# Optimization experiments

Hardware: AMD Instinct MI355X
Metric: run time of the kernel (lower is better)

Reference implementation:

```python
import jax, jax.numpy as jnp
import numpy as np

B, L, C = 1, 4096, 1024
H = 16
D = C // H  # head_dim = 64


def setup_inputs() -> dict:
    key = jax.random.key(0)
    k1, k2, k3 = jax.random.split(key, 3)
    scale_in = 1.0 / np.sqrt(C)
    return {
        "x": jax.random.normal(k1, (B, L, C), dtype=jnp.float32),
        "Wqkv": jax.random.normal(k2, (C, 3 * C), dtype=jnp.float32) * scale_in,
        "bqkv": jnp.zeros((3 * C,), dtype=jnp.float32),
        "Wout": jax.random.normal(k3, (C, C), dtype=jnp.float32) * scale_in,
        "bout": jnp.zeros((C,), dtype=jnp.float32),
    }


def reference(x, Wqkv, bqkv, Wout, bout):
    Bx, Lx, Cx = x.shape
    qkv = x @ Wqkv + bqkv                             # [B, L, 3C]
    qkv = qkv.reshape(Bx, Lx, 3, H, D)
    qkv = jnp.transpose(qkv, (2, 0, 3, 1, 4))         # [3, B, H, L, D]
    q, k, v = qkv[0], qkv[1], qkv[2]
    scores = jnp.einsum("bhqd,bhkd->bhqk", q, k) / jnp.sqrt(jnp.float32(D))
    # causal mask: strictly upper triangle -> -inf
    causal = jnp.triu(jnp.ones((Lx, Lx), dtype=bool), k=1)
    scores = jnp.where(causal, -jnp.inf, scores)
    attn = jax.nn.softmax(scores, axis=-1)            # [B, H, L, L]
    out = jnp.einsum("bhqk,bhkd->bhqd", attn, v)      # [B, H, L, D]
    out = jnp.transpose(out, (0, 2, 1, 3)).reshape(Bx, Lx, Cx)
    return out @ Wout + bout
```

## Files before the change

kernel.cpp:

```cpp
#include <hip/hip_runtime.h>
#include <hip/hip_bf16.h>

typedef unsigned short u16;
typedef __bf16 bf16x8 __attribute__((ext_vector_type(8)));
typedef float f32x4 __attribute__((ext_vector_type(4)));

#define L_SEQ 4096
#define CDIM  1024
#define NH    16
#define HD    64
#define N_QKV 3072
#define ATT_STRIDE 88

static __device__ __forceinline__ float bf2f(u16 u) {
    union { float f; unsigned int i; } v; v.i = ((unsigned int)u) << 16; return v.f;
}
static __device__ __forceinline__ u16 f2bf(float f) {
    union { float f; unsigned int i; } v; v.f = f;
    unsigned int u = v.i;
    return (u16)((u + 0x7fffu + ((u >> 16) & 1u)) >> 16);
}

static __device__ __forceinline__ f32x4 mfma16x16x32(bf16x8 a, bf16x8 b, f32x4 c) {
    return __builtin_amdgcn_mfma_f32_16x16x32_bf16(a, b, c, 0, 0, 0);
}

typedef const __attribute__((address_space(1))) unsigned int* gas_u32;
typedef __attribute__((address_space(3))) unsigned int* las_u32;
static __device__ __forceinline__ void gload_lds16(const u16* g, u16* l) {
    __builtin_amdgcn_global_load_lds((gas_u32)g, (las_u32)l, 16, 0, 0);
}

__global__ __launch_bounds__(256) void k_cast_x(const float* __restrict__ src,
                                                u16* __restrict__ dst, int n8) {
    int i = blockIdx.x * 256 + threadIdx.x;
    if (i >= n8) return;
    const float4* s = (const float4*)(src + (size_t)i * 8);
    float4 a = s[0], b = s[1];
    u16 o[8] = { f2bf(a.x), f2bf(a.y), f2bf(a.z), f2bf(a.w),
                 f2bf(b.x), f2bf(b.y), f2bf(b.z), f2bf(b.w) };
    *(uint4*)(dst + (size_t)i * 8) = *(uint4*)o;
}

__global__ __launch_bounds__(256) void k_transpose_cast(const float* __restrict__ src,
                                                        u16* __restrict__ dst,
                                                        int R, int C) {
    __shared__ u16 tile[32][33];
    int c0 = blockIdx.x * 32, r0 = blockIdx.y * 32;
    int tx = threadIdx.x & 31, ty = threadIdx.x >> 5;
#pragma unroll
    for (int i = 0; i < 32; i += 8)
        tile[ty + i][tx] = f2bf(src[(size_t)(r0 + ty + i) * C + c0 + tx]);
    __syncthreads();
#pragma unroll
    for (int i = 0; i < 32; i += 8)
        dst[(size_t)(c0 + ty + i) * R + r0 + tx] = tile[tx][ty + i];
}

__global__ __launch_bounds__(256) void k_transpose_v(const u16* __restrict__ qkv,
                                                     u16* __restrict__ vt) {
    __shared__ u16 tile[32][33];
    int k0 = blockIdx.x * 32, d0 = blockIdx.y * 32, h = blockIdx.z;
    int tx = threadIdx.x & 31, ty = threadIdx.x >> 5;
#pragma unroll
    for (int i = 0; i < 32; i += 8)
        tile[ty + i][tx] = qkv[(size_t)(k0 + ty + i) * N_QKV + 2 * CDIM + h * HD + d0 + tx];
    __syncthreads();
#pragma unroll
    for (int i = 0; i < 32; i += 8)
        vt[(size_t)(h * HD + d0 + ty + i) * L_SEQ + k0 + tx] = tile[tx][ty + i];
}

template <typename OutT>
__global__ __launch_bounds__(256) void k_gemm_bt(const u16* __restrict__ A,
                                                 const u16* __restrict__ Bt,
                                                 const float* __restrict__ bias,
                                                 OutT* __restrict__ Cmat,
                                                 int M, int N, int K) {
    __shared__ alignas(16) u16 As[128 * 32];
    __shared__ alignas(16) u16 Bs[128 * 32];
    int t = threadIdx.x;
    int n0 = blockIdx.x * 128, m0 = blockIdx.y * 128;
    int l = t & 63, w = t >> 6;
    int wm = (w >> 1) * 64, wn = (w & 1) * 64;
    int lr = l & 15, lq = l >> 4;

    const f32x4 vzero = {0.f, 0.f, 0.f, 0.f};
    f32x4 acc[4][4];
#pragma unroll
    for (int mi = 0; mi < 4; mi++)
#pragma unroll
        for (int ni = 0; ni < 4; ni++) acc[mi][ni] = vzero;

    int ar = t >> 2;
    int ac = (t & 3) * 8;
    const u16* Ag = A + (size_t)(m0 + ar) * K + ac;
    const u16* Bg = Bt + (size_t)(n0 + ar) * K + ac;
    u16* AsD0 = &As[t * 8];
    u16* AsD1 = &As[t * 8 + 64 * 32];
    u16* BsD0 = &Bs[t * 8];
    u16* BsD1 = &Bs[t * 8 + 64 * 32];

    for (int k0 = 0; k0 < K; k0 += 32) {
        gload_lds16(Ag + k0,                     AsD0);
        gload_lds16(Ag + (size_t)64 * K + k0,    AsD1);
        gload_lds16(Bg + k0,                     BsD0);
        gload_lds16(Bg + (size_t)64 * K + k0,    BsD1);
        __syncthreads();

        bf16x8 af[4], bfr[4];
#pragma unroll
        for (int mi = 0; mi < 4; mi++)
            af[mi] = *(const bf16x8*)&As[(wm + mi * 16 + lr) * 32 + lq * 8];
#pragma unroll
        for (int ni = 0; ni < 4; ni++)
            bfr[ni] = *(const bf16x8*)&Bs[(wn + ni * 16 + lr) * 32 + lq * 8];
#pragma unroll
        for (int mi = 0; mi < 4; mi++)
#pragma unroll
            for (int ni = 0; ni < 4; ni++)
                acc[mi][ni] = mfma16x16x32(af[mi], bfr[ni], acc[mi][ni]);
        __syncthreads();
    }

#pragma unroll
    for (int ni = 0; ni < 4; ni++) {
        int col = n0 + wn + ni * 16 + lr;
        float bv = bias[col];
#pragma unroll
        for (int mi = 0; mi < 4; mi++) {
            int row = m0 + wm + mi * 16 + lq * 4;
#pragma unroll
            for (int r = 0; r < 4; r++) {
                float v = acc[mi][ni][r] + bv;
                if constexpr (sizeof(OutT) == 2)
                    Cmat[(size_t)(row + r) * N + col] = f2bf(v);
                else
                    Cmat[(size_t)(row + r) * N + col] = v;
            }
        }
    }
}

__global__ __launch_bounds__(256) void k_attn(const u16* __restrict__ qkv,
                                              const u16* __restrict__ vt,
                                              u16* __restrict__ attn) {
    __shared__ alignas(16) u16 Ks[64 * ATT_STRIDE];
    __shared__ alignas(16) u16 Vs[64 * ATT_STRIDE];

    int t = threadIdx.x;
    int l = t & 63, w = t >> 6;
    int h = blockIdx.y;
    int lr = l & 15, lq = l >> 4;
    int row8 = t >> 3;
    int ch = (t & 7) * 8;
    int qloc = w * 16 + lr;

    const f32x4 vzero = {0.f, 0.f, 0.f, 0.f};
    const u16* Kbase = qkv + (size_t)row8 * N_QKV + CDIM + h * HD + ch;
    const u16* Vbase = vt + (size_t)(h * HD + row8) * L_SEQ + ch;

#pragma unroll
    for (int phase = 0; phase < 2; phase++) {
        int tile = phase ? (63 - blockIdx.x) : blockIdx.x;
        int q0 = tile * 64;
        int nkv = tile + 1;

        bf16x8 bq[2];
        {
            const u16* Qg = qkv + (size_t)(q0 + qloc) * N_QKV + h * HD + lq * 8;
            union { uint4 u; u16 hh[8]; } q0u, q1u;
            q0u.u = *(const uint4*)(Qg);
            q1u.u = *(const uint4*)(Qg + 32);
            union { bf16x8 v; u16 hh[8]; } f0, f1;
#pragma unroll
            for (int j = 0; j < 8; j++) {
                f0.hh[j] = f2bf(bf2f(q0u.hh[j]) * 0.125f);
                f1.hh[j] = f2bf(bf2f(q1u.hh[j]) * 0.125f);
            }
            bq[0] = f0.v; bq[1] = f1.v;
        }

        f32x4 o[4];
#pragma unroll
        for (int dt = 0; dt < 4; dt++) o[dt] = vzero;
        float m_i = -1e30f, l_i = 0.f;

        uint4 rk0, rk1, rv0, rv1;
        {
            const u16* Kg = Kbase;
            rk0 = *(const uint4*)Kg;
            rk1 = *(const uint4*)(Kg + (size_t)32 * N_QKV);
            const u16* Vg = Vbase;
            rv0 = *(const uint4*)Vg;
            rv1 = *(const uint4*)(Vg + (size_t)32 * L_SEQ);
        }

        for (int it = 0; it < nkv; ++it) {
            *(uint4*)&Ks[row8 * ATT_STRIDE + ch]        = rk0;
            *(uint4*)&Ks[(row8 + 32) * ATT_STRIDE + ch] = rk1;
            *(uint4*)&Vs[row8 * ATT_STRIDE + ch]        = rv0;
            *(uint4*)&Vs[(row8 + 32) * ATT_STRIDE + ch] = rv1;
            __syncthreads();

            if (it + 1 < nkv) {
                int k1 = (it + 1) * 64;
                const u16* Kg = Kbase + (size_t)k1 * N_QKV;
                rk0 = *(const uint4*)Kg;
                rk1 = *(const uint4*)(Kg + (size_t)32 * N_QKV);
                const u16* Vg = Vbase + k1;
                rv0 = *(const uint4*)Vg;
                rv1 = *(const uint4*)(Vg + (size_t)32 * L_SEQ);
            }

            f32x4 s[4];
#pragma unroll
            for (int nt = 0; nt < 4; nt++) s[nt] = vzero;
#pragma unroll
            for (int ks = 0; ks < 2; ks++)
#pragma unroll
                for (int nt = 0; nt < 4; nt++) {
                    bf16x8 ak = *(const bf16x8*)&Ks[(nt * 16 + lr) * ATT_STRIDE + ks * 32 + lq * 8];
                    s[nt] = mfma16x16x32(ak, bq[ks], s[nt]);
                }

            bool diag = ((it * 64) == q0);
            float tmax = -1e30f;
#pragma unroll
            for (int nt = 0; nt < 4; nt++)
#pragma unroll
                for (int r = 0; r < 4; r++) {
                    float v = s[nt][r];
                    if (diag && (nt * 16 + lq * 4 + r > qloc)) v = -1e30f;
                    s[nt][r] = v;
                    tmax = fmaxf(tmax, v);
                }
            tmax = fmaxf(tmax, __shfl_xor(tmax, 16));
            tmax = fmaxf(tmax, __shfl_xor(tmax, 32));

            float mnew = fmaxf(m_i, tmax);
            float alpha = __expf(m_i - mnew);
            float rsum = 0.f;
#pragma unroll
            for (int nt = 0; nt < 4; nt++)
#pragma unroll
                for (int r = 0; r < 4; r++) {
                    float e = __expf(s[nt][r] - mnew);
                    s[nt][r] = e;
                    rsum += e;
                }
            rsum += __shfl_xor(rsum, 16);
            rsum += __shfl_xor(rsum, 32);
            l_i = l_i * alpha + rsum;
            m_i = mnew;
#pragma unroll
            for (int dt = 0; dt < 4; dt++)
#pragma unroll
                for (int r = 0; r < 4; r++) o[dt][r] *= alpha;

#pragma unroll
            for (int a = 0; a < 2; a++) {
                union { bf16x8 v; u16 hh[8]; } bp;
#pragma unroll
                for (int r = 0; r < 4; r++) {
                    bp.hh[r]     = f2bf(s[2 * a][r]);
                    bp.hh[r + 4] = f2bf(s[2 * a + 1][r]);
                }
#pragma unroll
                for (int dt = 0; dt < 4; dt++) {
                    union { bf16x8 v; uint2 u2[2]; } av;
                    const u16* vrow = &Vs[(dt * 16 + lr) * ATT_STRIDE + a * 32 + lq * 4];
                    av.u2[0] = *(const uint2*)(vrow);
                    av.u2[1] = *(const uint2*)(vrow + 16);
                    o[dt] = mfma16x16x32(av.v, bp.v, o[dt]);
                }
            }
            __syncthreads();
        }

        float inv = 1.0f / l_i;
        int qg = q0 + qloc;
#pragma unroll
        for (int dt = 0; dt < 4; dt++) {
            union { u16 hh[4]; uint2 u2; } eo;
#pragma unroll
            for (int r = 0; r < 4; r++) eo.hh[r] = f2bf(o[dt][r] * inv);
            *(uint2*)&attn[(size_t)qg * CDIM + h * HD + dt * 16 + lq * 4] = eo.u2;
        }
    }
}

extern "C" void kernel_launch(void* const* d_in, const int* in_sizes, int n_in,
                              void* d_out, int out_size, void* d_ws, size_t ws_size,
                              hipStream_t stream) {
    const float* x    = (const float*)d_in[0];
    const float* Wqkv = (const float*)d_in[1];
    const float* bqkv = (const float*)d_in[2];
    const float* Wout = (const float*)d_in[3];
    const float* bout = (const float*)d_in[4];
    float* out = (float*)d_out;

    char* ws = (char*)d_ws;
    u16* qkv   = (u16*)(ws);
    u16* xb    = (u16*)(ws + 25165824);
    u16* attn  = xb;
    u16* vt    = (u16*)(ws + 33554432);
    u16* wqkvt = (u16*)(ws + 41943040);
    u16* woutt = (u16*)(ws + 48234496);

    k_cast_x<<<dim3(2048), 256, 0, stream>>>(x, xb, 524288);
    k_transpose_cast<<<dim3(96, 32), 256, 0, stream>>>(Wqkv, wqkvt, 1024, 3072);
    k_transpose_cast<<<dim3(32, 32), 256, 0, stream>>>(Wout, woutt, 1024, 1024);
    k_gemm_bt<u16><<<dim3(24, 32), 256, 0, stream>>>(xb, wqkvt, bqkv, qkv, 4096, 3072, 1024);
    k_transpose_v<<<dim3(128, 2, 16), 256, 0, stream>>>(qkv, vt);
    k_attn<<<dim3(32, 16), 256, 0, stream>>>(qkv, vt, attn);
    k_gemm_bt<float><<<dim3(8, 32), 256, 0, stream>>>(attn, woutt, bout, out, 4096, 1024, 1024);
}
```

Measured before the change: 246.9 us.

## Split attention KV range across two warp groups and merge softmax partials

The attention kernel now launches 512 threads per block. Two groups of four waves each process half of the KV tiles for the same query tile, each with its own shared-memory K/V buffers. The partial max, sum and output accumulators are then merged through shared memory in a flash-decoding style combine. This doubles the parallelism per query tile, since the grid of 512 blocks underfills the GPU. The cost is an extra merge step, block-wide syncs shared by both groups, and idle iterations for the group with fewer tiles.

After: 236.6 us. 1.04x faster.

```diff
diff --git a/kernel.cpp b/kernel.cpp
--- a/kernel.cpp
+++ b/kernel.cpp
@@ -142,29 +142,37 @@
     }
 }
 
-__global__ __launch_bounds__(256) void k_attn(const u16* __restrict__ qkv,
-                                              const u16* __restrict__ vt,
-                                              u16* __restrict__ attn) {
-    __shared__ alignas(16) u16 Ks[64 * ATT_STRIDE];
-    __shared__ alignas(16) u16 Vs[64 * ATT_STRIDE];
+__global__ __launch_bounds__(512, 4) void k_attn(const u16* __restrict__ qkv,
+                                                 const u16* __restrict__ vt,
+                                                 u16* __restrict__ attn) {
+    __shared__ alignas(16) u16 Ks[2][64 * ATT_STRIDE];
+    __shared__ alignas(16) u16 Vs[2][64 * ATT_STRIDE];
 
     int t = threadIdx.x;
     int l = t & 63, w = t >> 6;
+    int g = w >> 2;
+    int ww = w & 3;
     int h = blockIdx.y;
     int lr = l & 15, lq = l >> 4;
-    int row8 = t >> 3;
-    int ch = (t & 7) * 8;
-    int qloc = w * 16 + lr;
+    int tg = t & 255;
+    int row8 = tg >> 3;
+    int ch = (tg & 7) * 8;
+    int qloc = ww * 16 + lr;
 
     const f32x4 vzero = {0.f, 0.f, 0.f, 0.f};
     const u16* Kbase = qkv + (size_t)row8 * N_QKV + CDIM + h * HD + ch;
     const u16* Vbase = vt + (size_t)(h * HD + row8) * L_SEQ + ch;
+    u16* KsG = Ks[g];
+    u16* VsG = Vs[g];
 
 #pragma unroll
     for (int phase = 0; phase < 2; phase++) {
         int tile = phase ? (63 - blockIdx.x) : blockIdx.x;
         int q0 = tile * 64;
         int nkv = tile + 1;
+        int h0 = (nkv + 1) >> 1;
+        int myBeg = g ? h0 : 0;
+        int myCnt = g ? (nkv - h0) : h0;
 
         bf16x8 bq[2];
         {
@@ -186,25 +194,28 @@
         for (int dt = 0; dt < 4; dt++) o[dt] = vzero;
         float m_i = -1e30f, l_i = 0.f;
 
-        uint4 rk0, rk1, rv0, rv1;
-        {
-            const u16* Kg = Kbase;
+        uint4 rk0 = {0,0,0,0}, rk1 = {0,0,0,0}, rv0 = {0,0,0,0}, rv1 = {0,0,0,0};
+        if (myCnt > 0) {
+            const u16* Kg = Kbase + (size_t)(myBeg * 64) * N_QKV;
             rk0 = *(const uint4*)Kg;
             rk1 = *(const uint4*)(Kg + (size_t)32 * N_QKV);
-            const u16* Vg = Vbase;
+            const u16* Vg = Vbase + myBeg * 64;
             rv0 = *(const uint4*)Vg;
             rv1 = *(const uint4*)(Vg + (size_t)32 * L_SEQ);
         }
 
-        for (int it = 0; it < nkv; ++it) {
-            *(uint4*)&Ks[row8 * ATT_STRIDE + ch]        = rk0;
-            *(uint4*)&Ks[(row8 + 32) * ATT_STRIDE + ch] = rk1;
-            *(uint4*)&Vs[row8 * ATT_STRIDE + ch]        = rv0;
-            *(uint4*)&Vs[(row8 + 32) * ATT_STRIDE + ch] = rv1;
+        for (int it = 0; it < h0; ++it) {
+            bool act = it < myCnt;
+            if (act) {
+                *(uint4*)&KsG[row8 * ATT_STRIDE + ch]        = rk0;
+                *(uint4*)&KsG[(row8 + 32) * ATT_STRIDE + ch] = rk1;
+                *(uint4*)&VsG[row8 * ATT_STRIDE + ch]        = rv0;
+                *(uint4*)&VsG[(row8 + 32) * ATT_STRIDE + ch] = rv1;
+            }
             __syncthreads();
 
-            if (it + 1 < nkv) {
-                int k1 = (it + 1) * 64;
+            if (it + 1 < myCnt) {
+                int k1 = (myBeg + it + 1) * 64;
                 const u16* Kg = Kbase + (size_t)k1 * N_QKV;
                 rk0 = *(const uint4*)Kg;
                 rk1 = *(const uint4*)(Kg + (size_t)32 * N_QKV);
@@ -213,80 +224,111 @@
                 rv1 = *(const uint4*)(Vg + (size_t)32 * L_SEQ);
             }
 
-            f32x4 s[4];
-#pragma unroll
-            for (int nt = 0; nt < 4; nt++) s[nt] = vzero;
-#pragma unroll
-            for (int ks = 0; ks < 2; ks++)
-#pragma unroll
-                for (int nt = 0; nt < 4; nt++) {
-                    bf16x8 ak = *(const bf16x8*)&Ks[(nt * 16 + lr) * ATT_STRIDE + ks * 32 + lq * 8];
-                    s[nt] = mfma16x16x32(ak, bq[ks], s[nt]);
+            if (act) {
+                f32x4 s[4];
+#pragma unroll
+                for (int nt = 0; nt < 4; nt++) s[nt] = vzero;
+#pragma unroll
+                for (int ks = 0; ks < 2; ks++)
+#pragma unroll
+                    for (int nt = 0; nt < 4; nt++) {
+                        bf16x8 ak = *(const bf16x8*)&KsG[(nt * 16 + lr) * ATT_STRIDE + ks * 32 + lq * 8];
+                        s[nt] = mfma16x16x32(ak, bq[ks], s[nt]);
+                    }
+
+                bool diag = (((myBeg + it) * 64) == q0);
+                float tmax = -1e30f;
+#pragma unroll
+                for (int nt = 0; nt < 4; nt++)
+#pragma unroll
+                    for (int r = 0; r < 4; r++) {
+                        float v = s[nt][r];
+                        if (diag && (nt * 16 + lq * 4 + r > qloc)) v = -1e30f;
+                        s[nt][r] = v;
+                        tmax = fmaxf(tmax, v);
+                    }
+                tmax = fmaxf(tmax, __shfl_xor(tmax, 16));
+                tmax = fmaxf(tmax, __shfl_xor(tmax, 32));
+
+                float mnew = fmaxf(m_i, tmax);
+                float alpha = __expf(m_i - mnew);
+                float rsum = 0.f;
+#pragma unroll
+                for (int nt = 0; nt < 4; nt++)
+#pragma unroll
+                    for (int r = 0; r < 4; r++) {
+                        float e = __expf(s[nt][r] - mnew);
+                        s[nt][r] = e;
+                        rsum += e;
+                    }
+                rsum += __shfl_xor(rsum, 16);
+                rsum += __shfl_xor(rsum, 32);
+                l_i = l_i * alpha + rsum;
+                m_i = mnew;
+#pragma unroll
+                for (int dt = 0; dt < 4; dt++)
+#pragma unroll
+                    for (int r = 0; r < 4; r++) o[dt][r] *= alpha;
+
+#pragma unroll
+                for (int a = 0; a < 2; a++) {
+                    union { bf16x8 v; u16 hh[8]; } bp;
+#pragma unroll
+                    for (int r = 0; r < 4; r++) {
+                        bp.hh[r]     = f2bf(s[2 * a][r]);
+                        bp.hh[r + 4] = f2bf(s[2 * a + 1][r]);
+                    }
+#pragma unroll
+                    for (int dt = 0; dt < 4; dt++) {
+                        union { bf16x8 v; uint2 u2[2]; } av;
+                        const u16* vrow = &VsG[(dt * 16 + lr) * ATT_STRIDE + a * 32 + lq * 4];
+                        av.u2[0] = *(const uint2*)(vrow);
+                        av.u2[1] = *(const uint2*)(vrow + 16);
+                        o[dt] = mfma16x16x32(av.v, bp.v, o[dt]);
+                    }
                 }
-
-            bool diag = ((it * 64) == q0);
-            float tmax = -1e30f;
-#pragma unroll
-            for (int nt = 0; nt < 4; nt++)
-#pragma unroll
-                for (int r = 0; r < 4; r++) {
-                    float v = s[nt][r];
-                    if (diag && (nt * 16 + lq * 4 + r > qloc)) v = -1e30f;
-                    s[nt][r] = v;
-                    tmax = fmaxf(tmax, v);
-                }
-            tmax = fmaxf(tmax, __shfl_xor(tmax, 16));
-            tmax = fmaxf(tmax, __shfl_xor(tmax, 32));
-
-            float mnew = fmaxf(m_i, tmax);
-            float alpha = __expf(m_i - mnew);
-            float rsum = 0.f;
-#pragma unroll
-            for (int nt = 0; nt < 4; nt++)
-#pragma unroll
-                for (int r = 0; r < 4; r++) {
-                    float e = __expf(s[nt][r] - mnew);
-                    s[nt][r] = e;
-                    rsum += e;
-                }
-            rsum += __shfl_xor(rsum, 16);
-            rsum += __shfl_xor(rsum, 32);
-            l_i = l_i * alpha + rsum;
-            m_i = mnew;
-#pragma unroll
-            for (int dt = 0; dt < 4; dt++)
-#pragma unroll
-                for (int r = 0; r < 4; r++) o[dt][r] *= alpha;
-
-#pragma unroll
-            for (int a = 0; a < 2; a++) {
-                union { bf16x8 v; u16 hh[8]; } bp;
-#pragma unroll
-                for (int r = 0; r < 4; r++) {
-                    bp.hh[r]     = f2bf(s[2 * a][r]);
-                    bp.hh[r + 4] = f2bf(s[2 * a + 1][r]);
-                }
-#pragma unroll
-                for (int dt = 0; dt < 4; dt++) {
-                    union { bf16x8 v; uint2 u2[2]; } av;
-                    const u16* vrow = &Vs[(dt * 16 + lr) * ATT_STRIDE + a * 32 + lq * 4];
-                    av.u2[0] = *(const uint2*)(vrow);
-                    av.u2[1] = *(const uint2*)(vrow + 16);
-                    o[dt] = mfma16x16x32(av.v, bp.v, o[dt]);
-                }
             }
             __syncthreads();
         }
 
-        float inv = 1.0f / l_i;
-        int qg = q0 + qloc;
-#pragma unroll
-        for (int dt = 0; dt < 4; dt++) {
-            union { u16 hh[4]; uint2 u2; } eo;
-#pragma unroll
-            for (int r = 0; r < 4; r++) eo.hh[r] = f2bf(o[dt][r] * inv);
-            *(uint2*)&attn[(size_t)qg * CDIM + h * HD + dt * 16 + lq * 4] = eo.u2;
-        }
+        float* mb1 = (float*)Ks[1];
+        float* mb2 = (float*)Vs[1];
+        if (g == 1) {
+            float* p = mb1 + tg * 10;
+            p[0] = m_i; p[1] = l_i;
+#pragma unroll
+            for (int r = 0; r < 4; r++) { p[2 + r] = o[0][r]; p[6 + r] = o[1][r]; }
+            float* p2 = mb2 + tg * 8;
+#pragma unroll
+            for (int r = 0; r < 4; r++) { p2[r] = o[2][r]; p2[4 + r] = o[3][r]; }
+        }
+        __syncthreads();
+        if (g == 0) {
+            float* p = mb1 + tg * 10;
+            float m1v = p[0], l1v = p[1];
+            float mnew = fmaxf(m_i, m1v);
+            float a0 = __expf(m_i - mnew);
+            float a1 = __expf(m1v - mnew);
+            float lm = l_i * a0 + l1v * a1;
+            float* p2 = mb2 + tg * 8;
+            f32x4 o1[4];
+#pragma unroll
+            for (int r = 0; r < 4; r++) {
+                o1[0][r] = p[2 + r]; o1[1][r] = p[6 + r];
+                o1[2][r] = p2[r];    o1[3][r] = p2[4 + r];
+            }
+            float inv = 1.0f / lm;
+            int qg = q0 + qloc;
+#pragma unroll
+            for (int dt = 0; dt < 4; dt++) {
+                union { u16 hh[4]; uint2 u2; } eo;
+#pragma unroll
+                for (int r = 0; r < 4; r++)
+                    eo.hh[r] = f2bf((o[dt][r] * a0 + o1[dt][r] * a1) * inv);
+                *(uint2*)&attn[(size_t)qg * CDIM + h * HD + dt * 16 + lq * 4] = eo.u2;
+            }
+        }
+        __syncthreads();
     }
 }
 
@@ -313,6 +355,6 @@
     k_transpose_cast<<<dim3(32, 32), 256, 0, stream>>>(Wout, woutt, 1024, 1024);
     k_gemm_bt<u16><<<dim3(24, 32), 256, 0, stream>>>(xb, wqkvt, bqkv, qkv, 4096, 3072, 1024);
     k_transpose_v<<<dim3(128, 2, 16), 256, 0, stream>>>(qkv, vt);
-    k_attn<<<dim3(32, 16), 256, 0, stream>>>(qkv, vt, attn);
+    k_attn<<<dim3(32, 16), 512, 0, stream>>>(qkv, vt, attn);
     k_gemm_bt<float><<<dim3(8, 32), 256, 0, stream>>>(attn, woutt, bout, out, 4096, 1024, 1024);
 }
```
